# Kernel optimization log

Measured on AMD Instinct MI355X. Metric: run time of the kernel, lower is better.

Reference implementation:

```python
import jax, jax.numpy as jnp
import numpy as np

B, R, H = 64, 32, 1024  # batch, num_rounds, lstm_hidden_size
IN = 2 * H              # GatedTrans in_dim
EPS = 1e-12             # F.normalize eps


def _gated(x, Wy, by, Wg, bg):
    # GatedTrans: tanh branch * leaky_relu branch (slope 0.01, torch default)
    return jnp.tanh(x @ Wy + by) * jax.nn.leaky_relu(x @ Wg + bg, 0.01)


def setup_inputs() -> dict:
    key = jax.random.key(0)
    ks = jax.random.split(key, 12)
    s_in = 1.0 / np.sqrt(IN)
    s_h = 1.0 / np.sqrt(H)
    return {
        "hist": jax.random.normal(ks[0], (B, R, IN), jnp.float32),
        "ques": jax.random.normal(ks[1], (B, R, IN), jnp.float32),
        "W_hy": jax.random.normal(ks[2], (IN, H), jnp.float32) * s_in,
        "b_hy": jnp.zeros((H,), jnp.float32),
        "W_hg": jax.random.normal(ks[3], (IN, H), jnp.float32) * s_in,
        "b_hg": jnp.zeros((H,), jnp.float32),
        "W_qy": jax.random.normal(ks[4], (IN, H), jnp.float32) * s_in,
        "b_qy": jnp.zeros((H,), jnp.float32),
        "W_qg": jax.random.normal(ks[5], (IN, H), jnp.float32) * s_in,
        "b_qg": jnp.zeros((H,), jnp.float32),
        "W_att": jax.random.normal(ks[6], (H,), jnp.float32) * s_h,
        "b_att": jnp.zeros((), jnp.float32),
    }


def reference(hist, ques, W_hy, b_hy, W_hg, b_hg, W_qy, b_qy, W_qg, b_qg, W_att, b_att):
    hist_embed = _gated(hist, W_hy, b_hy, W_hg, b_hg)   # [B, R, H]
    ques_embed = _gated(ques, W_qy, b_qy, W_qg, b_qg)   # [B, R, H]
    # broadcast outer product over rounds: [B, Rq, Rh, H]
    att_embed = ques_embed[:, :, None, :] * hist_embed[:, None, :, :]
    norm = jnp.sqrt(jnp.sum(att_embed * att_embed, axis=-1, keepdims=True))
    att_embed = att_embed / jnp.maximum(norm, EPS)       # F.normalize(p=2)
    scores = att_embed @ W_att + b_att                   # [B, Rq, Rh]
    att = jax.nn.softmax(scores, axis=-1)
    tril = jnp.tril(jnp.ones((R, R), jnp.float32))       # causal round mask
    att_masked = att * tril
    att_masked = att_masked / jnp.sum(att_masked, axis=-1, keepdims=True)
    # weighted sum over hist rounds: [B, Rq, 2H]
    feat = jnp.einsum("bqh,bhd->bqd", att_masked, hist)
    return feat
```

## Files before the change

### kernel.cpp

```cpp
#include <hip/hip_runtime.h>
#include <cstdint>

#define IN_DIM 2048
#define H_DIM  1024
#define BROWS  2048
#define BATCH  64
#define ROUNDS 32

typedef __bf16 bf16x8 __attribute__((ext_vector_type(8)));
typedef float  f32x4  __attribute__((ext_vector_type(4)));
typedef unsigned short u16;

__device__ __forceinline__ u16 f2bf(float f) {
    unsigned int u = __float_as_uint(f);
    u += 0x7FFFu + ((u >> 16) & 1u);
    return (u16)(u >> 16);
}

__device__ __forceinline__ void async_ld16(const void* g, void* l) {
    __builtin_amdgcn_global_load_lds(
        (__attribute__((address_space(1))) void*)(uintptr_t)g,
        (__attribute__((address_space(3))) void*)(unsigned int)(uintptr_t)l,
        16, 0, 0);
}

#define BAR()    asm volatile("s_barrier" ::: "memory")
#define LGKM0()  asm volatile("s_waitcnt lgkmcnt(0)" ::: "memory")
#define VMCNT6() asm volatile("s_waitcnt vmcnt(6)" ::: "memory")
#define VMCNT0() asm volatile("s_waitcnt vmcnt(0)" ::: "memory")

__global__ __launch_bounds__(256) void prep(
    const float* __restrict__ hist, const float* __restrict__ ques,
    u16* __restrict__ xh, u16* __restrict__ xq,
    const float* __restrict__ why, const float* __restrict__ whg,
    const float* __restrict__ wqy, const float* __restrict__ wqg,
    u16* __restrict__ oh, u16* __restrict__ oq)
{
    int idx = blockIdx.x;
    if (idx < 4096) {
        int i = idx * 256 + threadIdx.x;
        const float4* h4 = (const float4*)hist;
        const float4* q4 = (const float4*)ques;
        float4 a = h4[i], b = q4[i];
        ushort4 oa, ob;
        oa.x = f2bf(a.x); oa.y = f2bf(a.y); oa.z = f2bf(a.z); oa.w = f2bf(a.w);
        ob.x = f2bf(b.x); ob.y = f2bf(b.y); ob.z = f2bf(b.z); ob.w = f2bf(b.w);
        ((ushort4*)xh)[i] = oa;
        ((ushort4*)xq)[i] = ob;
        return;
    }
    __shared__ float t[32][33];
    int zz = idx - 4096;
    int z = zz >> 12, rem = zz & 4095;
    const float* Y = z == 0 ? why : wqy;
    const float* G = z == 0 ? whg : wqg;
    u16* O = z == 0 ? oh : oq;
    int n0 = (rem & 63) * 32, k0 = (rem >> 6) * 32;
    int tx = threadIdx.x & 31, ty = threadIdx.x >> 5;
    const float* S = (tx < 16) ? Y : G;
    int sc = (n0 >> 1) + (tx & 15);
    #pragma unroll
    for (int r = 0; r < 4; r++)
        t[ty + 8*r][tx] = S[(size_t)(k0 + ty + 8*r) * H_DIM + sc];
    __syncthreads();
    #pragma unroll
    for (int r = 0; r < 4; r++)
        O[(size_t)(n0 + ty + 8*r) * IN_DIM + k0 + tx] = f2bf(t[tx][ty + 8*r]);
}

__global__ __launch_bounds__(512, 2) void gemm_act(
    const u16* __restrict__ xh, const u16* __restrict__ xq,
    const u16* __restrict__ wth, const u16* __restrict__ wtq,
    const float* __restrict__ bhy, const float* __restrict__ bhg,
    const float* __restrict__ bqy, const float* __restrict__ bqg,
    u16* __restrict__ eh, u16* __restrict__ eq)
{
    int L = blockIdx.x;
    int cluster = L & 7;
    int slot = L >> 3;
    int z = cluster >> 2;
    int y = (cluster & 1) * 4 + (slot >> 3);
    int x = ((cluster >> 1) & 1) * 8 + (slot & 7);
    int m0 = y * 256, n0 = x * 128;

    const u16* A  = z == 0 ? xh : xq;
    const u16* Bt = z == 0 ? wth : wtq;
    const float* by = z == 0 ? bhy : bqy;
    const float* bg = z == 0 ? bhg : bqg;
    u16* E = z == 0 ? eh : eq;

    __shared__ __align__(16) u16 As[2][256 * 64];
    __shared__ __align__(16) u16 Bs[2][128 * 64];

    int tid = threadIdx.x;
    int wave = tid >> 6, lane = tid & 63;
    int lane15 = lane & 15, quad = lane >> 4;
    int wm = (wave & 3) * 64;
    int wn = (wave >> 2) * 64;

    f32x4 acc[4][4];
    #pragma unroll
    for (int i = 0; i < 4; i++)
        #pragma unroll
        for (int j = 0; j < 4; j++) acc[i][j] = (f32x4){0.f, 0.f, 0.f, 0.f};

    int sArow[4], sAkc[4], sAcb[4];
    #pragma unroll
    for (int r2 = 0; r2 < 4; r2++) {
        int cbase = r2 * 512 + wave * 64;
        int cs = cbase + lane;
        int row = cs >> 3, s = cs & 7;
        sArow[r2] = row; sAkc[r2] = s ^ (row & 7); sAcb[r2] = cbase;
    }
    int sBrow[2], sBkc[2], sBcb[2];
    #pragma unroll
    for (int r2 = 0; r2 < 2; r2++) {
        int cbase = r2 * 512 + wave * 64;
        int cs = cbase + lane;
        int row = cs >> 3, s = cs & 7;
        sBrow[r2] = row; sBkc[r2] = s ^ (row & 7); sBcb[r2] = cbase;
    }

    #define STAGE(buf, kt)                                                                    \
        _Pragma("unroll")                                                                     \
        for (int r2 = 0; r2 < 4; r2++)                                                        \
            async_ld16(A + (size_t)(m0 + sArow[r2]) * IN_DIM + (kt) + sAkc[r2] * 8,           \
                       &As[buf][sAcb[r2] * 8]);                                               \
        _Pragma("unroll")                                                                     \
        for (int r2 = 0; r2 < 2; r2++)                                                        \
            async_ld16(Bt + (size_t)(n0 + sBrow[r2]) * IN_DIM + (kt) + sBkc[r2] * 8,          \
                       &Bs[buf][sBcb[r2] * 8]);

    bf16x8 af[2][4], bfv[2][4];

    #define READF(buf)                                                                        \
        _Pragma("unroll")                                                                     \
        for (int ks = 0; ks < 2; ks++) {                                                      \
            _Pragma("unroll")                                                                 \
            for (int i = 0; i < 4; i++) {                                                     \
                int row = wm + i * 16 + lane15;                                               \
                int s = (ks * 4 + quad) ^ (row & 7);                                          \
                af[ks][i] = *(const bf16x8*)&As[buf][row * 64 + s * 8];                       \
                int rowb = wn + i * 16 + lane15;                                              \
                int sb = (ks * 4 + quad) ^ (rowb & 7);                                        \
                bfv[ks][i] = *(const bf16x8*)&Bs[buf][rowb * 64 + sb * 8];                    \
            }                                                                                 \
        }

    #define DOMFMA()                                                                          \
        __builtin_amdgcn_s_setprio(1);                                                        \
        _Pragma("unroll")                                                                     \
        for (int ks = 0; ks < 2; ks++)                                                        \
            _Pragma("unroll")                                                                 \
            for (int i = 0; i < 4; i++)                                                       \
                _Pragma("unroll")                                                             \
                for (int j = 0; j < 4; j++)                                                   \
                    acc[i][j] = __builtin_amdgcn_mfma_f32_16x16x32_bf16(                      \
                        af[ks][i], bfv[ks][j], acc[i][j], 0, 0, 0);                           \
        __builtin_amdgcn_s_setprio(0);

    STAGE(0, 0)
    STAGE(1, 64)
    VMCNT6(); BAR();

    #pragma unroll 1
    for (int kt = 0; kt < IN_DIM; kt += 128) {
        READF(0)
        if (kt + 128 < IN_DIM) { LGKM0(); BAR(); STAGE(0, kt + 128) }
        DOMFMA()
        if (kt + 128 < IN_DIM) { VMCNT6(); } else { VMCNT0(); }
        BAR();
        READF(1)
        if (kt + 192 < IN_DIM) { LGKM0(); BAR(); STAGE(1, kt + 192) }
        DOMFMA()
        if (kt + 128 < IN_DIM) {
            if (kt + 192 < IN_DIM) { VMCNT6(); } else { VMCNT0(); }
            BAR();
        }
    }
    #undef STAGE
    #undef READF
    #undef DOMFMA

    int n0w = n0 + wn;
    #pragma unroll
    for (int jp = 0; jp < 2; jp++) {
        int hc = (n0w >> 1) + jp * 16 + lane15;
        float vy = by[hc], vg = bg[hc];
        #pragma unroll
        for (int i = 0; i < 4; i++) {
            #pragma unroll
            for (int r = 0; r < 4; r++) {
                int row = m0 + wm + i * 16 + quad * 4 + r;
                float y2 = tanhf(acc[i][2 * jp][r] + vy);
                float g = acc[i][2 * jp + 1][r] + vg;
                E[(size_t)row * H_DIM + hc] = f2bf(y2 * (g > 0.f ? g : 0.01f * g));
            }
        }
    }
}

__global__ __launch_bounds__(256) void score_feat(
    const u16* __restrict__ eh, const u16* __restrict__ eq,
    const float* __restrict__ hist, const float* __restrict__ watt,
    const float* __restrict__ batt, float* __restrict__ out)
{
    int idx = blockIdx.x;
    int b = idx & 63, q = idx >> 6;
    int tid = threadIdx.x, wave = tid >> 6, lane = tid & 63;
    __shared__ float sw[32], swn[32];

    const u16* qe = eq + (size_t)(b * ROUNDS + q) * H_DIM;
    float uw[16], u2[16];
    #pragma unroll
    for (int c = 0; c < 2; c++) {
        uint4 pk = ((const uint4*)qe)[lane + 64 * c];
        float4 w0 = ((const float4*)watt)[(lane + 64 * c) * 2];
        float4 w1 = ((const float4*)watt)[(lane + 64 * c) * 2 + 1];
        unsigned int ws[4] = {pk.x, pk.y, pk.z, pk.w};
        float wf[8] = {w0.x, w0.y, w0.z, w0.w, w1.x, w1.y, w1.z, w1.w};
        #pragma unroll
        for (int e = 0; e < 4; e++) {
            float lo = __uint_as_float(ws[e] << 16);
            float hi = __uint_as_float(ws[e] & 0xFFFF0000u);
            uw[c * 8 + 2 * e]     = lo * wf[2 * e];
            u2[c * 8 + 2 * e]     = lo * lo;
            uw[c * 8 + 2 * e + 1] = hi * wf[2 * e + 1];
            u2[c * 8 + 2 * e + 1] = hi * hi;
        }
    }
    for (int h = wave; h <= q; h += 4) {
        const u16* he = eh + (size_t)(b * ROUNDS + h) * H_DIM;
        float num = 0.f, nrm = 0.f;
        #pragma unroll
        for (int c = 0; c < 2; c++) {
            uint4 pk = ((const uint4*)he)[lane + 64 * c];
            unsigned int vs[4] = {pk.x, pk.y, pk.z, pk.w};
            #pragma unroll
            for (int e = 0; e < 4; e++) {
                float lo = __uint_as_float(vs[e] << 16);
                float hi = __uint_as_float(vs[e] & 0xFFFF0000u);
                num += uw[c * 8 + 2 * e] * lo + uw[c * 8 + 2 * e + 1] * hi;
                nrm += u2[c * 8 + 2 * e] * lo * lo + u2[c * 8 + 2 * e + 1] * hi * hi;
            }
        }
        #pragma unroll
        for (int off = 32; off > 0; off >>= 1) {
            num += __shfl_down(num, off);
            nrm += __shfl_down(nrm, off);
        }
        if (lane == 0)
            sw[h] = num / fmaxf(sqrtf(nrm), 1e-12f) + batt[0];
    }
    __syncthreads();
    if (tid == 0) {
        float mx = -1e30f;
        for (int h = 0; h <= q; h++) mx = fmaxf(mx, sw[h]);
        float zs = 0.f;
        for (int h = 0; h <= q; h++) { float e = expf(sw[h] - mx); swn[h] = e; zs += e; }
        float inv = 1.f / zs;
        for (int h = 0; h <= q; h++) swn[h] *= inv;
    }
    __syncthreads();
    const float4* hb = (const float4*)(hist + (size_t)b * ROUNDS * IN_DIM);
    float4* ob = (float4*)(out + (size_t)(b * ROUNDS + q) * IN_DIM);
    #pragma unroll
    for (int d0 = 0; d0 < 2; d0++) {
        int d = tid + d0 * 256;
        float4 a = {0.f, 0.f, 0.f, 0.f};
        for (int h = 0; h <= q; h++) {
            float w = swn[h];
            float4 x = hb[h * 512 + d];
            a.x += w * x.x; a.y += w * x.y; a.z += w * x.z; a.w += w * x.w;
        }
        ob[d] = a;
    }
}

extern "C" void kernel_launch(void* const* d_in, const int* in_sizes, int n_in,
                              void* d_out, int out_size, void* d_ws, size_t ws_size,
                              hipStream_t stream) {
    const float* hist = (const float*)d_in[0];
    const float* ques = (const float*)d_in[1];
    const float* Why  = (const float*)d_in[2];
    const float* bhy  = (const float*)d_in[3];
    const float* Whg  = (const float*)d_in[4];
    const float* bhg  = (const float*)d_in[5];
    const float* Wqy  = (const float*)d_in[6];
    const float* bqy  = (const float*)d_in[7];
    const float* Wqg  = (const float*)d_in[8];
    const float* bqg  = (const float*)d_in[9];
    const float* watt = (const float*)d_in[10];
    const float* batt = (const float*)d_in[11];
    float* out = (float*)d_out;

    char* w = (char*)d_ws;
    u16* Xh  = (u16*)w;
    u16* Xq  = Xh  + (size_t)BROWS * IN_DIM;
    u16* WtH = Xq  + (size_t)BROWS * IN_DIM;
    u16* WtQ = WtH + (size_t)IN_DIM * IN_DIM;
    u16* Eh  = WtQ + (size_t)IN_DIM * IN_DIM;
    u16* Eq  = Eh  + (size_t)BROWS * H_DIM;

    prep<<<12288, 256, 0, stream>>>(hist, ques, Xh, Xq, Why, Whg, Wqy, Wqg, WtH, WtQ);
    gemm_act<<<256, 512, 0, stream>>>(Xh, Xq, WtH, WtQ, bhy, bhg, bqy, bqg, Eh, Eq);
    score_feat<<<2048, 256, 0, stream>>>(Eh, Eq, hist, watt, batt, out);
}
```

Baseline: 183.0 us.

## Double-buffer LDS fragment registers to overlap ds_reads with MFMA in GEMM loop

Splits each 64-wide K tile into two half-steps with separate register fragment sets (a0/b0, a1/b1). The next half-step's LDS reads are issued before the current MFMA block, so LDS read latency is hidden behind matrix math instead of being fully exposed before each MFMA batch. Barrier and global-to-LDS staging points are moved to fit the new schedule. The trade-offs are more live registers, which can lower occupancy, and global-load waits placed sooner after staging, which could expose memory latency.

New measurement: 187.3 us. 1.02x slower.

```diff
diff --git a/kernel.cpp b/kernel.cpp
--- a/kernel.cpp
+++ b/kernel.cpp
@@ -131,56 +131,57 @@
             async_ld16(Bt + (size_t)(n0 + sBrow[r2]) * IN_DIM + (kt) + sBkc[r2] * 8,          \
                        &Bs[buf][sBcb[r2] * 8]);
 
-    bf16x8 af[2][4], bfv[2][4];
-
-    #define READF(buf)                                                                        \
+    bf16x8 a0[4], b0[4], a1[4], b1[4];
+
+    #define DSREAD(da, db, buf, ks)                                                           \
         _Pragma("unroll")                                                                     \
-        for (int ks = 0; ks < 2; ks++) {                                                      \
-            _Pragma("unroll")                                                                 \
-            for (int i = 0; i < 4; i++) {                                                     \
-                int row = wm + i * 16 + lane15;                                               \
-                int s = (ks * 4 + quad) ^ (row & 7);                                          \
-                af[ks][i] = *(const bf16x8*)&As[buf][row * 64 + s * 8];                       \
-                int rowb = wn + i * 16 + lane15;                                              \
-                int sb = (ks * 4 + quad) ^ (rowb & 7);                                        \
-                bfv[ks][i] = *(const bf16x8*)&Bs[buf][rowb * 64 + sb * 8];                    \
-            }                                                                                 \
-        }
-
-    #define DOMFMA()                                                                          \
+        for (int i = 0; i < 4; i++) {                                                         \
+            int row = wm + i * 16 + lane15;                                                   \
+            int s = ((ks) * 4 + quad) ^ (row & 7);                                            \
+            da[i] = *(const bf16x8*)&As[buf][row * 64 + s * 8];                               \
+            int rowb = wn + i * 16 + lane15;                                                  \
+            int sb = ((ks) * 4 + quad) ^ (rowb & 7);                                          \
+            db[i] = *(const bf16x8*)&Bs[buf][rowb * 64 + sb * 8];                             \
+        }
+
+    #define MFMA16(fa, fb)                                                                    \
         __builtin_amdgcn_s_setprio(1);                                                        \
         _Pragma("unroll")                                                                     \
-        for (int ks = 0; ks < 2; ks++)                                                        \
+        for (int i = 0; i < 4; i++)                                                           \
             _Pragma("unroll")                                                                 \
-            for (int i = 0; i < 4; i++)                                                       \
-                _Pragma("unroll")                                                             \
-                for (int j = 0; j < 4; j++)                                                   \
-                    acc[i][j] = __builtin_amdgcn_mfma_f32_16x16x32_bf16(                      \
-                        af[ks][i], bfv[ks][j], acc[i][j], 0, 0, 0);                           \
+            for (int j = 0; j < 4; j++)                                                       \
+                acc[i][j] = __builtin_amdgcn_mfma_f32_16x16x32_bf16(                          \
+                    fa[i], fb[j], acc[i][j], 0, 0, 0);                                        \
         __builtin_amdgcn_s_setprio(0);
 
     STAGE(0, 0)
     STAGE(1, 64)
     VMCNT6(); BAR();
+    DSREAD(a0, b0, 0, 0)
 
     #pragma unroll 1
     for (int kt = 0; kt < IN_DIM; kt += 128) {
-        READF(0)
-        if (kt + 128 < IN_DIM) { LGKM0(); BAR(); STAGE(0, kt + 128) }
-        DOMFMA()
-        if (kt + 128 < IN_DIM) { VMCNT6(); } else { VMCNT0(); }
+        DSREAD(a1, b1, 0, 1)
+        MFMA16(a0, b0)
+        LGKM0(); BAR();
+        if (kt + 128 < IN_DIM) { STAGE(0, kt + 128) VMCNT6(); }
+        else                   { VMCNT0(); }
         BAR();
-        READF(1)
-        if (kt + 192 < IN_DIM) { LGKM0(); BAR(); STAGE(1, kt + 192) }
-        DOMFMA()
+        DSREAD(a0, b0, 1, 0)
+        MFMA16(a1, b1)
+        DSREAD(a1, b1, 1, 1)
+        MFMA16(a0, b0)
         if (kt + 128 < IN_DIM) {
-            if (kt + 192 < IN_DIM) { VMCNT6(); } else { VMCNT0(); }
-            BAR();
-        }
+            LGKM0(); BAR();
+            STAGE(1, kt + 192)
+            VMCNT6(); BAR();
+            DSREAD(a0, b0, 0, 0)
+        }
+        MFMA16(a1, b1)
     }
     #undef STAGE
-    #undef READF
-    #undef DOMFMA
+    #undef DSREAD
+    #undef MFMA16
 
     int n0w = n0 + wn;
     #pragma unroll
```
